# Kernel optimization log

Measured on AMD Instinct MI355X. Metric: run time of the kernel, lower is better.

Reference implementation:

```python
import jax, jax.numpy as jnp
import numpy as np
import math


def setup_inputs() -> dict:
    key = jax.random.key(0)
    k1, k2 = jax.random.split(key)
    B, C, D = 16, 128, 8192
    x = jax.random.normal(k1, (B, C, D), dtype=jnp.float32)
    centers = jnp.linspace(-1.5, 1.5, 16, dtype=jnp.float32)
    widths = jnp.full((16,), 0.2, dtype=jnp.float32)
    return {"x": x, "centers": centers, "widths": widths}


def reference(x, centers, widths):
    # x: [B, C, D]; centers/widths: [nbins]
    B, C = x.shape[0], x.shape[1]
    xf = x.reshape(B * C, -1)                      # [N, D]
    # z: [N, nbins, D]
    z = (xf[:, None, :] - centers[None, :, None]) / widths[None, :, None]
    mean_exp = jnp.mean(jnp.exp(-0.5 * z * z), axis=-1)  # [N, nbins]
    coeff = 1.0 / (widths * jnp.sqrt(jnp.asarray(2.0 * math.pi, dtype=x.dtype)))
    res = coeff[None, :] * mean_exp                # [N, nbins]
    return res.reshape(B, -1)                      # [B, C*nbins]
```

## Files before the change

### kernel.cpp

```cpp
#include <hip/hip_runtime.h>
#include <math.h>

#define NB 16
#define BLOCK 256
#define DDIM 8192
#define NF 512
#define XLO (-4.0f)
#define FSCALE 64.0f
#define WPTS 128

#if __has_builtin(__builtin_amdgcn_exp2f)
#define EXP2(x) __builtin_amdgcn_exp2f(x)
#else
#define EXP2(x) exp2f(x)
#endif

#if __has_builtin(__builtin_amdgcn_fmed3f)
#define CLAMPF(x, lo, hi) __builtin_amdgcn_fmed3f((x), (lo), (hi))
#else
#define CLAMPF(x, lo, hi) fminf(fmaxf((x), (lo)), (hi))
#endif

__global__ __launch_bounds__(BLOCK) void hist_rows_kernel(
    const float* __restrict__ x,
    const float* __restrict__ centers,
    const float* __restrict__ widths,
    float* __restrict__ out) {
  __shared__ unsigned int hist[NF];

  const int row = blockIdx.x;
  const int tid = threadIdx.x;

  reinterpret_cast<uint2*>(hist)[tid] = make_uint2(0u, 0u);
  __syncthreads();

  const float4* xr = reinterpret_cast<const float4*>(x + (size_t)row * DDIM);
#pragma unroll
  for (int it = 0; it < DDIM / (BLOCK * 4); ++it) {
    const float4 v = xr[it * BLOCK + tid];
    const float e4[4] = {v.x, v.y, v.z, v.w};
#pragma unroll
    for (int k = 0; k < 4; ++k) {
      float p = fmaf(e4[k], FSCALE, 256.5f);
      p = CLAMPF(p, 0.0f, (float)(NF - 1));
      const unsigned int i = (unsigned int)p;
      atomicAdd(&hist[i], 1u);
    }
  }
  __syncthreads();

  const int g = tid >> 4;
  const int l = tid & 15;
  const float w = widths[g];
  const float c = centers[g];
  const float A = -0.5f * 1.4426950408889634f / (w * w);

  int b0 = ((int)fmaf(c, FSCALE, (float)(NF / 2)) - WPTS / 2) & ~3;
  b0 = min(max(b0, 0), NF - WPTS);
  const float gx_base = XLO + (float)b0 * (1.0f / FSCALE);

  float s = 0.0f;
#pragma unroll
  for (int k = 0; k < WPTS / 64; ++k) {
    const int boff = k * 64 + l * 4;
    const uint4 h = *reinterpret_cast<const uint4*>(&hist[b0 + boff]);
    const float d0 = (gx_base - c) + (float)boff * (1.0f / FSCALE);
    const float d1 = d0 + 1.0f / FSCALE;
    const float d2 = d0 + 2.0f / FSCALE;
    const float d3 = d0 + 3.0f / FSCALE;
    s = fmaf((float)h.x, EXP2((A * d0) * d0), s);
    s = fmaf((float)h.y, EXP2((A * d1) * d1), s);
    s = fmaf((float)h.z, EXP2((A * d2) * d2), s);
    s = fmaf((float)h.w, EXP2((A * d3) * d3), s);
  }

  s += __shfl_xor(s, 1, 16);
  s += __shfl_xor(s, 2, 16);
  s += __shfl_xor(s, 4, 16);
  s += __shfl_xor(s, 8, 16);

  if (l == 0) {
    const float coeff = 1.0f / (w * 2.5066282746310002f);
    out[(size_t)row * NB + g] = s * coeff * (1.0f / (float)DDIM);
  }
}

extern "C" void kernel_launch(void* const* d_in, const int* in_sizes, int n_in,
                              void* d_out, int out_size, void* d_ws, size_t ws_size,
                              hipStream_t stream) {
  const float* x = (const float*)d_in[0];
  const float* centers = (const float*)d_in[1];
  const float* widths = (const float*)d_in[2];
  float* out = (float*)d_out;

  const int nrows = out_size / NB;
  hist_rows_kernel<<<nrows, BLOCK, 0, stream>>>(x, centers, widths, out);
}
```

Baseline: 17.25 us.

## Process two rows per block, prefetching the second row during the first histogram

Each block now handles two rows. It loads row A, then issues the loads for row B before building row A's histogram and its Gaussian reduction, using a separate shared histogram buffer for each row. This hides global memory latency behind the atomic and exp work and amortizes block setup. The cost is a grid half the size and extra registers holding the prefetched data, which may lower occupancy.

```diff
diff --git a/kernel.cpp b/kernel.cpp
--- a/kernel.cpp
+++ b/kernel.cpp
@@ -8,6 +8,7 @@
 #define XLO (-4.0f)
 #define FSCALE 64.0f
 #define WPTS 128
+#define ITERS (DDIM / (BLOCK * 4))
 
 #if __has_builtin(__builtin_amdgcn_exp2f)
 #define EXP2(x) __builtin_amdgcn_exp2f(x)
@@ -26,25 +27,33 @@
     const float* __restrict__ centers,
     const float* __restrict__ widths,
     float* __restrict__ out) {
-  __shared__ unsigned int hist[NF];
+  __shared__ unsigned int hist[2][NF];
 
-  const int row = blockIdx.x;
+  const int row0 = blockIdx.x * 2;
   const int tid = threadIdx.x;
 
-  reinterpret_cast<uint2*>(hist)[tid] = make_uint2(0u, 0u);
+  const float4* xrA = reinterpret_cast<const float4*>(x + (size_t)row0 * DDIM);
+  const float4* xrB = reinterpret_cast<const float4*>(x + (size_t)(row0 + 1) * DDIM);
+
+  float4 va[ITERS];
+#pragma unroll
+  for (int it = 0; it < ITERS; ++it) va[it] = xrA[it * BLOCK + tid];
+
+  reinterpret_cast<uint4*>(&hist[0][0])[tid] = make_uint4(0u, 0u, 0u, 0u);
   __syncthreads();
 
-  const float4* xr = reinterpret_cast<const float4*>(x + (size_t)row * DDIM);
+  float4 vb[ITERS];
 #pragma unroll
-  for (int it = 0; it < DDIM / (BLOCK * 4); ++it) {
-    const float4 v = xr[it * BLOCK + tid];
-    const float e4[4] = {v.x, v.y, v.z, v.w};
+  for (int it = 0; it < ITERS; ++it) vb[it] = xrB[it * BLOCK + tid];
+
+#pragma unroll
+  for (int it = 0; it < ITERS; ++it) {
+    const float e4[4] = {va[it].x, va[it].y, va[it].z, va[it].w};
 #pragma unroll
     for (int k = 0; k < 4; ++k) {
       float p = fmaf(e4[k], FSCALE, 256.5f);
       p = CLAMPF(p, 0.0f, (float)(NF - 1));
-      const unsigned int i = (unsigned int)p;
-      atomicAdd(&hist[i], 1u);
+      atomicAdd(&hist[0][(unsigned int)p], 1u);
     }
   }
   __syncthreads();
@@ -54,35 +63,62 @@
   const float w = widths[g];
   const float c = centers[g];
   const float A = -0.5f * 1.4426950408889634f / (w * w);
-
   int b0 = ((int)fmaf(c, FSCALE, (float)(NF / 2)) - WPTS / 2) & ~3;
   b0 = min(max(b0, 0), NF - WPTS);
   const float gx_base = XLO + (float)b0 * (1.0f / FSCALE);
+  const float coeff = 1.0f / (w * 2.5066282746310002f);
 
-  float s = 0.0f;
+  float sA = 0.0f;
 #pragma unroll
   for (int k = 0; k < WPTS / 64; ++k) {
     const int boff = k * 64 + l * 4;
-    const uint4 h = *reinterpret_cast<const uint4*>(&hist[b0 + boff]);
+    const uint4 h = *reinterpret_cast<const uint4*>(&hist[0][b0 + boff]);
     const float d0 = (gx_base - c) + (float)boff * (1.0f / FSCALE);
     const float d1 = d0 + 1.0f / FSCALE;
     const float d2 = d0 + 2.0f / FSCALE;
     const float d3 = d0 + 3.0f / FSCALE;
-    s = fmaf((float)h.x, EXP2((A * d0) * d0), s);
-    s = fmaf((float)h.y, EXP2((A * d1) * d1), s);
-    s = fmaf((float)h.z, EXP2((A * d2) * d2), s);
-    s = fmaf((float)h.w, EXP2((A * d3) * d3), s);
+    sA = fmaf((float)h.x, EXP2((A * d0) * d0), sA);
+    sA = fmaf((float)h.y, EXP2((A * d1) * d1), sA);
+    sA = fmaf((float)h.z, EXP2((A * d2) * d2), sA);
+    sA = fmaf((float)h.w, EXP2((A * d3) * d3), sA);
   }
+  sA += __shfl_xor(sA, 1, 16);
+  sA += __shfl_xor(sA, 2, 16);
+  sA += __shfl_xor(sA, 4, 16);
+  sA += __shfl_xor(sA, 8, 16);
+  if (l == 0) out[(size_t)row0 * NB + g] = sA * coeff * (1.0f / (float)DDIM);
 
-  s += __shfl_xor(s, 1, 16);
-  s += __shfl_xor(s, 2, 16);
-  s += __shfl_xor(s, 4, 16);
-  s += __shfl_xor(s, 8, 16);
+#pragma unroll
+  for (int it = 0; it < ITERS; ++it) {
+    const float e4[4] = {vb[it].x, vb[it].y, vb[it].z, vb[it].w};
+#pragma unroll
+    for (int k = 0; k < 4; ++k) {
+      float p = fmaf(e4[k], FSCALE, 256.5f);
+      p = CLAMPF(p, 0.0f, (float)(NF - 1));
+      atomicAdd(&hist[1][(unsigned int)p], 1u);
+    }
+  }
+  __syncthreads();
 
-  if (l == 0) {
-    const float coeff = 1.0f / (w * 2.5066282746310002f);
-    out[(size_t)row * NB + g] = s * coeff * (1.0f / (float)DDIM);
+  float sB = 0.0f;
+#pragma unroll
+  for (int k = 0; k < WPTS / 64; ++k) {
+    const int boff = k * 64 + l * 4;
+    const uint4 h = *reinterpret_cast<const uint4*>(&hist[1][b0 + boff]);
+    const float d0 = (gx_base - c) + (float)boff * (1.0f / FSCALE);
+    const float d1 = d0 + 1.0f / FSCALE;
+    const float d2 = d0 + 2.0f / FSCALE;
+    const float d3 = d0 + 3.0f / FSCALE;
+    sB = fmaf((float)h.x, EXP2((A * d0) * d0), sB);
+    sB = fmaf((float)h.y, EXP2((A * d1) * d1), sB);
+    sB = fmaf((float)h.z, EXP2((A * d2) * d2), sB);
+    sB = fmaf((float)h.w, EXP2((A * d3) * d3), sB);
   }
+  sB += __shfl_xor(sB, 1, 16);
+  sB += __shfl_xor(sB, 2, 16);
+  sB += __shfl_xor(sB, 4, 16);
+  sB += __shfl_xor(sB, 8, 16);
+  if (l == 0) out[(size_t)(row0 + 1) * NB + g] = sB * coeff * (1.0f / (float)DDIM);
 }
 
 extern "C" void kernel_launch(void* const* d_in, const int* in_sizes, int n_in,
@@ -94,5 +130,5 @@
   float* out = (float*)d_out;
 
   const int nrows = out_size / NB;
-  hist_rows_kernel<<<nrows, BLOCK, 0, stream>>>(x, centers, widths, out);
+  hist_rows_kernel<<<nrows / 2, BLOCK, 0, stream>>>(x, centers, widths, out);
 }
```

Result: no change. 17.30 us (+0.2%).
